# Kernel optimization log

Measured on AMD Instinct MI355X. Metric: run time of the kernel, lower is better.

Reference implementation:

```python
import jax, jax.numpy as jnp
import numpy as np

N_CORES = 64
N_QUBITS = 1024
QEMB = 256
N_EDGES = 448
BATCH = 512
NN_DIMS = (256, 512, 512, 256)


def setup_inputs() -> dict:
    key = jax.random.key(0)
    ks = jax.random.split(key, 12)
    inp = {
        "core_allocs": jax.random.randint(ks[0], (BATCH, N_QUBITS), 0, N_CORES, dtype=jnp.int32),
        "qubit_embs": jax.random.normal(ks[1], (N_QUBITS, QEMB), dtype=jnp.float32),
        "dummy_qubit_emb": jax.random.normal(ks[2], (QEMB,), dtype=jnp.float32),
        "edge_index": jax.random.randint(ks[3], (2, N_EDGES), 0, N_CORES, dtype=jnp.int32),
        "edge_weight": jax.random.uniform(ks[4], (N_EDGES,), dtype=jnp.float32),
        "W1": jax.random.normal(ks[5], (NN_DIMS[0], NN_DIMS[1]), dtype=jnp.float32) * 0.05,
        "b1": jax.random.normal(ks[6], (NN_DIMS[1],), dtype=jnp.float32) * 0.05,
        "W2": jax.random.normal(ks[7], (NN_DIMS[1], NN_DIMS[2]), dtype=jnp.float32) * 0.05,
        "b2": jax.random.normal(ks[8], (NN_DIMS[2],), dtype=jnp.float32) * 0.05,
        "W3": jax.random.normal(ks[9], (NN_DIMS[2], NN_DIMS[3]), dtype=jnp.float32) * 0.05,
        "b3": jax.random.normal(ks[10], (NN_DIMS[3],), dtype=jnp.float32) * 0.05,
    }
    return inp


def _gcn_norm(edge_index, edge_weight):
    # PyG gcn_norm: add self loops (weight 1), symmetric D^{-1/2} A D^{-1/2}.
    self_idx = jnp.arange(N_CORES, dtype=edge_index.dtype)
    row = jnp.concatenate([edge_index[0], self_idx])
    col = jnp.concatenate([edge_index[1], self_idx])
    w = jnp.concatenate([edge_weight, jnp.ones((N_CORES,), edge_weight.dtype)])
    deg = jax.ops.segment_sum(w, col, num_segments=N_CORES)  # degree at targets
    dinv = jnp.where(deg > 0, deg ** -0.5, 0.0)
    norm = dinv[row] * w * dinv[col]
    return row, col, norm


def reference(core_allocs, qubit_embs, dummy_qubit_emb, edge_index, edge_weight,
              W1, b1, W2, b2, W3, b3):
    # ---- unmixedCoreEmbs, vectorized: per-core max over assigned qubit embs,
    # dummy emb always included (cores never at capacity) ----
    def pool(alloc):  # alloc: [n_qubits] -> [n_cores, qemb]
        seg = jax.ops.segment_max(qubit_embs, alloc, num_segments=N_CORES)
        return jnp.maximum(seg, dummy_qubit_emb)  # also fixes -inf empty cores

    x = jax.vmap(pool)(core_allocs)  # [B, n_cores, qemb]

    # ---- GCNConv stack (same graph replicated per batch element) ----
    row, col, norm = _gcn_norm(edge_index, edge_weight)

    def gcn_layer(h, W, b):
        hw = h @ W  # [B, C, d_out]
        msg = hw[:, row, :] * norm[None, :, None]  # gather sources, scale
        agg = jnp.zeros((h.shape[0], N_CORES, W.shape[1]), hw.dtype).at[:, col, :].add(msg)
        return jax.nn.relu(agg + b)

    x = gcn_layer(x, W1, b1)
    x = gcn_layer(x, W2, b2)
    x = gcn_layer(x, W3, b3)
    return x  # [B, n_cores, nn_dims[-1]] (original returns this split per batch element)
```

## Files before the change

kernel.cpp:

```cpp
#include <hip/hip_runtime.h>
#include <type_traits>

typedef __attribute__((ext_vector_type(8))) short short8;
typedef __attribute__((ext_vector_type(4))) short short4v;
typedef __attribute__((ext_vector_type(2))) short short2v;
typedef __attribute__((ext_vector_type(4))) float f32x4;
typedef unsigned short u16;
typedef unsigned int u32;

#define N_EDGES 448

#define WS_ADJA 0
#define WS_ADJB 4096
#define WS_W1   8192
#define WS_W2   139264
#define WS_W3   401408
#define WS_DUM  532480
#define WS_B1   (WS_DUM + 256)
#define WS_B2   (WS_DUM + 768)
#define WS_B3   (WS_DUM + 1280)
#define WS_QE   534528
#define WS_FLAG 796672

__device__ __forceinline__ float bf2f(u16 v) {
    u32 u = ((u32)v) << 16;
    return __builtin_bit_cast(float, u);
}
__device__ __forceinline__ u16 f2bf(float f) {
    u32 u = __builtin_bit_cast(u32, f);
    u32 r = u + 0x7FFFu + ((u >> 16) & 1u);
    return (u16)(r >> 16);
}
__device__ __forceinline__ u16 f2bf_fast(float f) {
    u32 u = __builtin_bit_cast(u32, f);
    return (u16)((u + 0x8000u) >> 16);
}
__device__ __forceinline__ float ldf(const void* p, int idx, u32 isf32) {
    return isf32 ? ((const float*)p)[idx] : bf2f(((const u16*)p)[idx]);
}
__device__ __forceinline__ u16 keyb(u16 b) {
    return (u16)(b ^ ((u16)(((u16)((short)b >> 15)) >> 1)));
}
__device__ __forceinline__ u32 pkmax(u32 a, u32 b) {
    short2v x = __builtin_bit_cast(short2v, a);
    short2v y = __builtin_bit_cast(short2v, b);
    short2v r = __builtin_elementwise_max(x, y);
    return __builtin_bit_cast(u32, r);
}

__global__ __launch_bounds__(512) void prep(
    const int* __restrict__ eidx, const void* __restrict__ ew,
    const void* __restrict__ qembs, const void* __restrict__ dummy,
    const void* __restrict__ W1, const void* __restrict__ b1,
    const void* __restrict__ W2, const void* __restrict__ b2,
    const void* __restrict__ W3, const void* __restrict__ b3,
    u16* __restrict__ ws) {
    const int t = threadIdx.x, bb = blockIdx.x;
    __shared__ u32 s_isf;
    if (t < 64) {
        const u16* qs = (const u16*)qembs;
        int c = 0;
#pragma unroll
        for (int j = 0; j < 4; j++) {
            u16 v = qs[(t * 4 + j) * 2];
            u32 e = (v >> 7) & 0xFF;
            c += (e >= 100 && e <= 134) ? 1 : 0;
        }
#pragma unroll
        for (int off = 32; off > 0; off >>= 1) c += __shfl_down(c, off, 64);
        if (t == 0) s_isf = (c < 128) ? 1u : 0u;
    }
    __syncthreads();
    const u32 isf32 = s_isf;

    if (t < 128) {
        const int bw = bb * 2 + (t >> 6);
        const int tl = t & 63;
        const void* src;
        int N, K32, dst, nt, kk, l2;
        if (bw < 256)      { src = W1; N = 512; K32 = 8;  dst = WS_W1; nt = bw / 8;          kk = bw % 8;         l2 = 2; }
        else if (bw < 768) { src = W2; N = 512; K32 = 16; dst = WS_W2; nt = (bw - 256) / 16; kk = (bw - 256) % 16; l2 = 2; }
        else               { src = W3; N = 256; K32 = 16; dst = WS_W3; nt = (bw - 768) / 16; kk = (bw - 768) % 16; l2 = 1; }
        const int col = nt * 16 + (tl & 15);
        const int krow = kk * 32 + (tl >> 4) * 8;
        u16 v[8];
#pragma unroll
        for (int j = 0; j < 8; j++) v[j] = f2bf(ldf(src, (krow + j) * N + col, isf32));
        const int chunk = ((((nt >> l2) * K32 + kk) << l2) | (nt & ((1 << l2) - 1)));
        u16* o = ws + dst + chunk * 512 + tl * 8;
#pragma unroll
        for (int j = 0; j < 8; j++) o[j] = v[j];
    }
    if (t >= 256) {
        const int base = bb * 512 + (t - 256) * 2;
        ws[WS_QE + base]     = keyb(f2bf(ldf(qembs, base, isf32)));
        ws[WS_QE + base + 1] = keyb(f2bf(ldf(qembs, base + 1, isf32)));
    }
    if (bb == 1) {
#pragma unroll
        for (int j = 0; j < 4; j++) {
            int i = t + j * 512;
            if (i < 1792) {
                u16 o;
                if (i < 256)       o = keyb(f2bf(ldf(dummy, i, isf32)));
                else if (i < 768)  o = f2bf(ldf(b1, i - 256, isf32));
                else if (i < 1280) o = f2bf(ldf(b2, i - 768, isf32));
                else               o = f2bf(ldf(b3, i - 1280, isf32));
                ws[WS_DUM + i] = o;
            }
        }
    }
    if (bb == 0) {
        __shared__ float A[4096];
        __shared__ float deg[64];
        __shared__ float dinv[64];
        __shared__ int er[N_EDGES];
        __shared__ int ec[N_EDGES];
        __shared__ float ewf[N_EDGES];
        if (t < N_EDGES) {
            er[t] = eidx[t];
            ec[t] = eidx[N_EDGES + t];
            ewf[t] = ldf(ew, t, isf32);
        }
        if (t < 64) deg[t] = 1.0f;
        for (int i = t; i < 4096; i += 512) A[i] = 0.f;
        __syncthreads();
        if (t < N_EDGES) atomicAdd(&deg[ec[t]], ewf[t]);
        __syncthreads();
        if (t < 64) dinv[t] = 1.0f / sqrtf(deg[t]);
        __syncthreads();
        if (t < N_EDGES) atomicAdd(&A[ec[t] * 64 + er[t]], dinv[er[t]] * ewf[t] * dinv[ec[t]]);
        __syncthreads();
        if (t < 64) A[t * 64 + t] += dinv[t] * dinv[t];
        __syncthreads();
        for (int i = t; i < 4096; i += 512) {
            int chunk = i >> 9, m = (i >> 3) & 63, j = i & 7;
            ws[WS_ADJA + i] = f2bf(A[m * 64 + chunk * 8 + j]);
        }
        for (int i = t; i < 4096; i += 512) {
            int chunk = i >> 9, l = (i >> 3) & 63, j = i & 7;
            int ntc = chunk >> 1, kk = chunk & 1;
            int k = kk * 32 + (l >> 4) * 8 + j;
            int c2 = ntc * 16 + (l & 15);
            ws[WS_ADJB + i] = f2bf(A[c2 * 64 + k]);
        }
        if (t == 0) *(u32*)(ws + WS_FLAG) = isf32;
    }
}

__global__ __launch_bounds__(512, 4) void fused(
    const int* __restrict__ allocs, const u16* __restrict__ ws,
    void* __restrict__ out) {

    __shared__ __align__(16) u16 BUF[64 * 512];
    __shared__ __align__(16) u16 ADJB_S[4096];

    const int t = threadIdx.x, bb = blockIdx.x;
    const int wave = t >> 6, lane = t & 63, quad = lane >> 4, nl = lane & 15;
    const u32 isf32 = *(const u32*)(ws + WS_FLAG);

    *(uint4*)(ADJB_S + t * 8) = *(const uint4*)(ws + WS_ADJB + t * 8);

    {
        int* LIST = (int*)(BUF + 16384);
        int* CNT  = LIST + 1024;
        int* SST  = CNT + 64;
        int* WOF  = SST + 64;
        if (t < 64) CNT[t] = 0;
        __syncthreads();
        const int c0 = allocs[bb * 1024 + t];
        const int c1 = allocs[bb * 1024 + 512 + t];
        atomicAdd(&CNT[c0], 1);
        atomicAdd(&CNT[c1], 1);
        __syncthreads();
        if (t < 64) {
            int v = CNT[t], s = v;
#pragma unroll
            for (int off = 1; off < 64; off <<= 1) {
                int u = __shfl_up(s, off, 64);
                if (t >= off) s += u;
            }
            SST[t] = s - v;
            WOF[t] = s - v;
        }
        __syncthreads();
        {
            int p0 = atomicAdd(&WOF[c0], 1); LIST[p0] = t;
            int p1 = atomicAdd(&WOF[c1], 1); LIST[p1] = 512 + t;
        }
        __syncthreads();
        const u16* wsq = ws + WS_QE;
        const uint2 dk = *(const uint2*)(ws + WS_DUM + lane * 4);
        for (int i = 0; i < 8; i++) {
            const int c = wave * 8 + i;
            const int L = CNT[c], S = SST[c];
            u32 m0 = dk.x, m1 = dk.y;
            int j = 0;
            for (; j + 4 <= L; j += 4) {
                const int q0 = LIST[S + j],     q1 = LIST[S + j + 1];
                const int q2 = LIST[S + j + 2], q3 = LIST[S + j + 3];
                uint2 ra = *(const uint2*)(wsq + q0 * 256 + lane * 4);
                uint2 rb = *(const uint2*)(wsq + q1 * 256 + lane * 4);
                uint2 rc = *(const uint2*)(wsq + q2 * 256 + lane * 4);
                uint2 rd = *(const uint2*)(wsq + q3 * 256 + lane * 4);
                m0 = pkmax(pkmax(m0, ra.x), pkmax(rb.x, rc.x));
                m1 = pkmax(pkmax(m1, ra.y), pkmax(rb.y, rc.y));
                m0 = pkmax(m0, rd.x);
                m1 = pkmax(m1, rd.y);
            }
            for (; j < L; j++) {
                const int q = LIST[S + j];
                uint2 r = *(const uint2*)(wsq + q * 256 + lane * 4);
                m0 = pkmax(m0, r.x);
                m1 = pkmax(m1, r.y);
            }
            short4v p;
            p[0] = (short)keyb((u16)(m0 & 0xffffu));
            p[1] = (short)keyb((u16)(m0 >> 16));
            p[2] = (short)keyb((u16)(m1 & 0xffffu));
            p[3] = (short)keyb((u16)(m1 >> 16));
            *(short4v*)(BUF + (lane >> 1) * 512 + c * 8 + (lane & 1) * 4) = p;
        }
    }
    __syncthreads();

    auto layerT = [&](auto K32c, const u16* __restrict__ W, const u16* __restrict__ bias) {
        constexpr int K32 = decltype(K32c)::value;
        const int s0 = wave * 4;
        u16* scr = BUF + (wave * 8 + 6) * 512;
        const u16* wp = W + (wave * K32 * 4) * 512 + lane * 8;
        f32x4 acc[4][4];
#pragma unroll
        for (int s = 0; s < 4; s++)
#pragma unroll
            for (int rt = 0; rt < 4; rt++) acc[s][rt] = f32x4{0.f, 0.f, 0.f, 0.f};
#pragma unroll 2
        for (int kk = 0; kk < K32; kk++) {
            short8 a[4];
#pragma unroll
            for (int rt = 0; rt < 4; rt++)
                a[rt] = *(const short8*)(BUF + (kk * 4 + quad) * 512 + (rt * 16 + nl) * 8);
            const u16* wk = wp + kk * 4 * 512;
            {
                short8 b0 = *(const short8*)(wk);
                short8 b1 = *(const short8*)(wk + 512);
#pragma unroll
                for (int rt = 0; rt < 4; rt++)
                    acc[0][rt] = __builtin_amdgcn_mfma_f32_16x16x32_bf16(a[rt], b0, acc[0][rt], 0, 0, 0);
#pragma unroll
                for (int rt = 0; rt < 4; rt++)
                    acc[1][rt] = __builtin_amdgcn_mfma_f32_16x16x32_bf16(a[rt], b1, acc[1][rt], 0, 0, 0);
            }
            {
                short8 b2 = *(const short8*)(wk + 1024);
                short8 b3 = *(const short8*)(wk + 1536);
#pragma unroll
                for (int rt = 0; rt < 4; rt++)
                    acc[2][rt] = __builtin_amdgcn_mfma_f32_16x16x32_bf16(a[rt], b2, acc[2][rt], 0, 0, 0);
#pragma unroll
                for (int rt = 0; rt < 4; rt++)
                    acc[3][rt] = __builtin_amdgcn_mfma_f32_16x16x32_bf16(a[rt], b3, acc[3][rt], 0, 0, 0);
            }
        }
        __syncthreads();
        short8 adjB0[4];
#pragma unroll
        for (int ntc = 0; ntc < 4; ntc++)
            adjB0[ntc] = *(const short8*)(ADJB_S + (ntc * 2) * 512 + lane * 8);
#pragma unroll
        for (int s = 0; s < 4; s++) {
            const int nt = s0 + s;
            float bv[4];
#pragma unroll
            for (int rr = 0; rr < 4; rr++) bv[rr] = bf2f(bias[nt * 16 + quad * 4 + rr]);
            f32x4 agg[4];
#pragma unroll
            for (int ntc = 0; ntc < 4; ntc++) agg[ntc] = f32x4{0.f, 0.f, 0.f, 0.f};
#pragma unroll
            for (int h = 0; h < 2; h++) {
#pragma unroll
                for (int r2 = 0; r2 < 2; r2++) {
                    f32x4 v = acc[s][2 * h + r2];
                    short4v p;
#pragma unroll
                    for (int rr = 0; rr < 4; rr++) p[rr] = (short)f2bf_fast(v[rr]);
                    *(short4v*)(scr + nl * 40 + r2 * 16 + quad * 4) = p;
                }
                short8 hwf = *(const short8*)(scr + nl * 40 + quad * 8);
                if (h == 0) {
#pragma unroll
                    for (int ntc = 0; ntc < 4; ntc++)
                        agg[ntc] = __builtin_amdgcn_mfma_f32_16x16x32_bf16(hwf, adjB0[ntc], agg[ntc], 0, 0, 0);
                } else {
#pragma unroll
                    for (int ntc = 0; ntc < 4; ntc++) {
                        short8 bfrag = *(const short8*)(ADJB_S + (ntc * 2 + 1) * 512 + lane * 8);
                        agg[ntc] = __builtin_amdgcn_mfma_f32_16x16x32_bf16(hwf, bfrag, agg[ntc], 0, 0, 0);
                    }
                }
            }
#pragma unroll
            for (int ntc = 0; ntc < 4; ntc++) {
                short4v p;
#pragma unroll
                for (int rr = 0; rr < 4; rr++)
                    p[rr] = (short)f2bf_fast(fmaxf(agg[ntc][rr] + bv[rr], 0.f));
                *(short4v*)(BUF + (nt * 2 + (quad >> 1)) * 512 + (ntc * 16 + nl) * 8 + (quad & 1) * 4) = p;
            }
        }
        __syncthreads();
    };

    auto layer3 = [&](const u16* __restrict__ W) {
        const u16* wp = W + (wave * 16 * 2) * 512 + lane * 8;
        f32x4 acc[2][4];
#pragma unroll
        for (int s = 0; s < 2; s++)
#pragma unroll
            for (int rt = 0; rt < 4; rt++) acc[s][rt] = f32x4{0.f, 0.f, 0.f, 0.f};
#pragma unroll 2
        for (int kk = 0; kk < 16; kk++) {
            short8 a[4];
#pragma unroll
            for (int rt = 0; rt < 4; rt++)
                a[rt] = *(const short8*)(BUF + (kk * 4 + quad) * 512 + (rt * 16 + nl) * 8);
            const u16* wk = wp + kk * 2 * 512;
            short8 b0 = *(const short8*)(wk);
            short8 b1 = *(const short8*)(wk + 512);
#pragma unroll
            for (int rt = 0; rt < 4; rt++)
                acc[0][rt] = __builtin_amdgcn_mfma_f32_16x16x32_bf16(a[rt], b0, acc[0][rt], 0, 0, 0);
#pragma unroll
            for (int rt = 0; rt < 4; rt++)
                acc[1][rt] = __builtin_amdgcn_mfma_f32_16x16x32_bf16(a[rt], b1, acc[1][rt], 0, 0, 0);
        }
        __syncthreads();
        u16* scr = BUF + 16384 + wave * 640;
#pragma unroll
        for (int s = 0; s < 2; s++) {
            const int nt = wave * 2 + s;
#pragma unroll
            for (int h = 0; h < 2; h++) {
#pragma unroll
                for (int r2 = 0; r2 < 2; r2++) {
                    f32x4 v = acc[s][2 * h + r2];
                    short4v p;
#pragma unroll
                    for (int rr = 0; rr < 4; rr++) p[rr] = (short)f2bf_fast(v[rr]);
                    *(short4v*)(scr + nl * 40 + r2 * 16 + quad * 4) = p;
                }
                short8 hwf = *(const short8*)(scr + nl * 40 + quad * 8);
                *(short8*)(BUF + (nt * 2 + h) * 512 + lane * 8) = hwf;
            }
        }
        __syncthreads();
    };

    layerT(std::integral_constant<int, 8>{},  ws + WS_W1, ws + WS_B1);
    layerT(std::integral_constant<int, 16>{}, ws + WS_W2, ws + WS_B2);
    layer3(ws + WS_W3);

    {
        const int rt2 = wave & 3, nt0 = (wave >> 2) * 8;
        short8 aA[2];
#pragma unroll
        for (int h = 0; h < 2; h++)
            aA[h] = *(const short8*)(ws + WS_ADJA + (h * 4 + quad) * 512 + (rt2 * 16 + nl) * 8);
        f32x4 accv[8];
#pragma unroll
        for (int ni = 0; ni < 8; ni++) {
            const int nt = nt0 + ni;
            short8 b0v = *(const short8*)(BUF + (nt * 2 + 0) * 512 + lane * 8);
            short8 b1v = *(const short8*)(BUF + (nt * 2 + 1) * 512 + lane * 8);
            f32x4 a = f32x4{0.f, 0.f, 0.f, 0.f};
            a = __builtin_amdgcn_mfma_f32_16x16x32_bf16(aA[0], b0v, a, 0, 0, 0);
            a = __builtin_amdgcn_mfma_f32_16x16x32_bf16(aA[1], b1v, a, 0, 0, 0);
            accv[ni] = a;
        }
        if (isf32) {
            float* outf = (float*)out + (size_t)bb * 16384;
#pragma unroll
            for (int ni = 0; ni < 8; ni++) {
                const int n = (nt0 + ni) * 16 + nl;
                const float bv = bf2f(ws[WS_B3 + n]);
#pragma unroll
                for (int rr = 0; rr < 4; rr++) {
                    const int m2 = rt2 * 16 + quad * 4 + rr;
                    outf[m2 * 256 + n] = fmaxf(accv[ni][rr] + bv, 0.f);
                }
            }
        } else {
            u16* outu = (u16*)out + (size_t)bb * 16384;
#pragma unroll
            for (int ni = 0; ni < 8; ni++) {
                const int n = (nt0 + ni) * 16 + nl;
                const float bv = bf2f(ws[WS_B3 + n]);
#pragma unroll
                for (int rr = 0; rr < 4; rr++) {
                    const int m2 = rt2 * 16 + quad * 4 + rr;
                    outu[m2 * 256 + n] = f2bf_fast(fmaxf(accv[ni][rr] + bv, 0.f));
                }
            }
        }
    }
}

extern "C" void kernel_launch(void* const* d_in, const int* in_sizes, int n_in,
                              void* d_out, int out_size, void* d_ws, size_t ws_size,
                              hipStream_t stream) {
    const int* allocs = (const int*)d_in[0];
    const void* qembs = d_in[1];
    const void* dummy = d_in[2];
    const int* eidx   = (const int*)d_in[3];
    const void* ew    = d_in[4];
    const void* W1 = d_in[5];
    const void* b1 = d_in[6];
    const void* W2 = d_in[7];
    const void* b2 = d_in[8];
    const void* W3 = d_in[9];
    const void* b3 = d_in[10];
    u16* ws = (u16*)d_ws;

    prep<<<512, 512, 0, stream>>>(eidx, ew, qembs, dummy, W1, b1, W2, b2, W3, b3, ws);
    fused<<<512, 512, 0, stream>>>(allocs, ws, d_out);
}
```

Before: 140.0 us.

## Merge prep and fused kernels into one launch with a grid-wide barrier

Combines the weight/adjacency preparation kernel and the main fused GCN kernel into a single kernel, separated by a software grid barrier built from an atomic counter and a gate flag in workspace memory. A small memset resets the counter each call. The goal is to remove the second kernel launch and the gap between kernels. In exchange, 512 blocks must all be co-resident or the spin-wait deadlocks, and every block now waits for the slowest prep block.

```diff
diff --git a/kernel.cpp b/kernel.cpp
--- a/kernel.cpp
+++ b/kernel.cpp
@@ -9,6 +9,7 @@
 typedef unsigned int u32;
 
 #define N_EDGES 448
+#define NBLK 512
 
 #define WS_ADJA 0
 #define WS_ADJB 4096
@@ -21,6 +22,8 @@
 #define WS_B3   (WS_DUM + 1280)
 #define WS_QE   534528
 #define WS_FLAG 796672
+#define WS_CNT  796674
+#define WS_GATE 796676
 
 __device__ __forceinline__ float bf2f(u16 v) {
     u32 u = ((u32)v) << 16;
@@ -48,15 +51,22 @@
     return __builtin_bit_cast(u32, r);
 }
 
-__global__ __launch_bounds__(512) void prep(
+__global__ __launch_bounds__(512, 4) void fused_all(
+    const int* __restrict__ allocs,
     const int* __restrict__ eidx, const void* __restrict__ ew,
     const void* __restrict__ qembs, const void* __restrict__ dummy,
     const void* __restrict__ W1, const void* __restrict__ b1,
     const void* __restrict__ W2, const void* __restrict__ b2,
     const void* __restrict__ W3, const void* __restrict__ b3,
-    u16* __restrict__ ws) {
+    u16* __restrict__ ws, void* __restrict__ out) {
+
+    __shared__ __align__(16) u16 BUF[64 * 512];
+    __shared__ __align__(16) u16 ADJB_S[4096];
+    __shared__ u32 s_isf;
+
     const int t = threadIdx.x, bb = blockIdx.x;
-    __shared__ u32 s_isf;
+    const int wave = t >> 6, lane = t & 63, quad = lane >> 4, nl = lane & 15;
+
     if (t < 64) {
         const u16* qs = (const u16*)qembs;
         int c = 0;
@@ -111,12 +121,12 @@
         }
     }
     if (bb == 0) {
-        __shared__ float A[4096];
-        __shared__ float deg[64];
-        __shared__ float dinv[64];
-        __shared__ int er[N_EDGES];
-        __shared__ int ec[N_EDGES];
-        __shared__ float ewf[N_EDGES];
+        float* A    = (float*)BUF;
+        float* deg  = A + 4096;
+        float* dinv = deg + 64;
+        int*   er   = (int*)(dinv + 64);
+        int*   ec   = er + N_EDGES;
+        float* ewf  = (float*)(ec + N_EDGES);
         if (t < N_EDGES) {
             er[t] = eidx[t];
             ec[t] = eidx[N_EDGES + t];
@@ -146,18 +156,27 @@
         }
         if (t == 0) *(u32*)(ws + WS_FLAG) = isf32;
     }
-}
-
-__global__ __launch_bounds__(512, 4) void fused(
-    const int* __restrict__ allocs, const u16* __restrict__ ws,
-    void* __restrict__ out) {
-
-    __shared__ __align__(16) u16 BUF[64 * 512];
-    __shared__ __align__(16) u16 ADJB_S[4096];
-
-    const int t = threadIdx.x, bb = blockIdx.x;
-    const int wave = t >> 6, lane = t & 63, quad = lane >> 4, nl = lane & 15;
-    const u32 isf32 = *(const u32*)(ws + WS_FLAG);
+
+    {
+        u32* cnt  = (u32*)(ws + WS_CNT);
+        u32* gate = (u32*)(ws + WS_GATE);
+        __syncthreads();
+        __threadfence();
+        if (t == 0) {
+            u32 old = __hip_atomic_fetch_add(cnt, 1u, __ATOMIC_ACQ_REL,
+                                             __HIP_MEMORY_SCOPE_AGENT);
+            if (old == (u32)(NBLK - 1)) {
+                __hip_atomic_store(gate, 1u, __ATOMIC_RELEASE,
+                                   __HIP_MEMORY_SCOPE_AGENT);
+            } else {
+                while (__hip_atomic_load(gate, __ATOMIC_ACQUIRE,
+                                         __HIP_MEMORY_SCOPE_AGENT) == 0u)
+                    __builtin_amdgcn_s_sleep(2);
+            }
+        }
+        __syncthreads();
+        __threadfence();
+    }
 
     *(uint4*)(ADJB_S + t * 8) = *(const uint4*)(ws + WS_ADJB + t * 8);
 
@@ -421,6 +440,7 @@
     const void* b3 = d_in[10];
     u16* ws = (u16*)d_ws;
 
-    prep<<<512, 512, 0, stream>>>(eidx, ew, qembs, dummy, W1, b1, W2, b2, W3, b3, ws);
-    fused<<<512, 512, 0, stream>>>(allocs, ws, d_out);
-}
+    hipMemsetAsync((char*)d_ws + (size_t)WS_CNT * 2, 0, 8, stream);
+    fused_all<<<NBLK, 512, 0, stream>>>(allocs, eidx, ew, qembs, dummy,
+                                        W1, b1, W2, b2, W3, b3, ws, d_out);
+}
```

New measurement: 278.5 us. +98.9%, slower.
